# Kernel tuning notes

Hardware: AMD Instinct MI355X
Metric: run time of the kernel (lower is better)

Reference implementation:

```python
import jax, jax.numpy as jnp
import numpy as np

BLOCK = 16
NVFP4_LEVELS = jnp.array([0.0, 0.5, 1.0, 1.5, 2.0, 3.0, 4.0, 6.0], dtype=jnp.float32)


def _quantize_to_nvfp4(x_blocks):
    # x_blocks: [n_blocks, BLOCK]
    amax = jnp.clip(jnp.max(jnp.abs(x_blocks), axis=-1, keepdims=True), 1e-12, None)
    scale = amax / 6.0
    x_norm = jnp.abs(x_blocks) / scale
    idx = jnp.argmin(jnp.abs(x_norm[..., None] - NVFP4_LEVELS), axis=-1)
    return jnp.sign(x_blocks) * NVFP4_LEVELS[idx] * scale


def setup_inputs() -> dict:
    key = jax.random.key(0)
    k1, k2, k3, k4 = jax.random.split(key, 4)
    B, S, H, O = 16, 1024, 1152, 4608
    x = jax.random.normal(k1, (B, S, H), dtype=jnp.float32)
    w_quantized = jax.random.normal(k2, (O, H), dtype=jnp.float32) * 0.02
    smooth_scale = jax.random.uniform(k3, (H,), dtype=jnp.float32, minval=0.5, maxval=2.0)
    bias = jax.random.normal(k4, (O,), dtype=jnp.float32) * 0.02
    return {"x": x, "w_quantized": w_quantized, "smooth_scale": smooth_scale, "bias": bias}


def reference(x, w_quantized, smooth_scale, bias):
    orig_shape = x.shape
    H = orig_shape[-1]
    # SmoothQuant activation prescale
    x_s = (x * smooth_scale).reshape(-1, H)              # [T, H]
    # per-token prescale to [-6, 6]
    token_max = jnp.clip(jnp.max(jnp.abs(x_s), axis=-1, keepdims=True), 1e-12, None)
    pre_scale = token_max / 6.0
    x_pre = x_s / pre_scale
    # blockwise NVFP4 fake quant
    x_q = _quantize_to_nvfp4(x_pre.reshape(-1, BLOCK)).reshape(x_s.shape)
    x_q = x_q * pre_scale                                # restore token scale
    out = x_q.reshape(orig_shape) @ w_quantized.T + bias  # F.linear
    return out
```

## Files before the change

### kernel.cpp

```cpp
#include <hip/hip_runtime.h>
#include <hip/hip_bf16.h>

typedef __attribute__((ext_vector_type(8))) _Float16 f16x8;
typedef __attribute__((ext_vector_type(4))) float  f32x4;

#define H_DIM 1152
#define H_VEC (H_DIM / 4)

__device__ __forceinline__ float nvfp4_level(float xn) {
    return xn <= 0.25f ? 0.0f
         : xn <= 0.75f ? 0.5f
         : xn <= 1.25f ? 1.0f
         : xn <= 1.75f ? 1.5f
         : xn <= 2.5f  ? 2.0f
         : xn <= 3.5f  ? 3.0f
         : xn <= 5.0f  ? 4.0f : 6.0f;
}

__global__ __launch_bounds__(256) void quant_kernel(
    const float4* __restrict__ x4, const float4* __restrict__ s4,
    _Float16* __restrict__ xq)
{
    const int t    = (blockIdx.x << 2) + (threadIdx.x >> 6);
    const int lane = threadIdx.x & 63;
    const float4* xrow = x4 + (size_t)t * H_VEC;

    float4 v[5];
    int    fidx[5];
    float  m = 0.f;
    #pragma unroll
    for (int i = 0; i < 5; ++i) {
        const int f = (i < 4) ? (lane + 64 * i) : (256 + (lane & 31));
        fidx[i] = f;
        const float4 xx = xrow[f];
        const float4 ss = s4[f];
        float4 vv;
        vv.x = xx.x * ss.x; vv.y = xx.y * ss.y;
        vv.z = xx.z * ss.z; vv.w = xx.w * ss.w;
        v[i] = vv;
        m = fmaxf(m, fmaxf(fmaxf(fabsf(vv.x), fabsf(vv.y)),
                           fmaxf(fabsf(vv.z), fabsf(vv.w))));
    }
    #pragma unroll
    for (int off = 32; off; off >>= 1)
        m = fmaxf(m, __shfl_xor(m, off, 64));
    const float pre_scale = fmaxf(m, 1e-12f) / 6.0f;

    #pragma unroll
    for (int i = 0; i < 5; ++i) {
        float4 p;
        p.x = v[i].x / pre_scale;
        p.y = v[i].y / pre_scale;
        p.z = v[i].z / pre_scale;
        p.w = v[i].w / pre_scale;
        float g = fmaxf(fmaxf(fabsf(p.x), fabsf(p.y)),
                        fmaxf(fabsf(p.z), fabsf(p.w)));
        g = fmaxf(g, __shfl_xor(g, 1, 64));
        g = fmaxf(g, __shfl_xor(g, 2, 64));
        const float scale = fmaxf(g, 1e-12f) / 6.0f;

        alignas(8) _Float16 o[4];
        {
            float q;
            q = copysignf(nvfp4_level(fabsf(p.x) / scale) * scale, p.x) * pre_scale;
            o[0] = (_Float16)q;
            q = copysignf(nvfp4_level(fabsf(p.y) / scale) * scale, p.y) * pre_scale;
            o[1] = (_Float16)q;
            q = copysignf(nvfp4_level(fabsf(p.z) / scale) * scale, p.z) * pre_scale;
            o[2] = (_Float16)q;
            q = copysignf(nvfp4_level(fabsf(p.w) / scale) * scale, p.w) * pre_scale;
            o[3] = (_Float16)q;
        }
        if (i < 4 || lane < 32) {
            _Float16* dst = xq + (size_t)t * H_DIM + fidx[i] * 4;
            *(uint2*)dst = *(const uint2*)o;
        }
    }
}

__global__ __launch_bounds__(256) void wconv_kernel(
    const float* __restrict__ w, _Float16* __restrict__ wq, int n)
{
    int i = (blockIdx.x * 256 + threadIdx.x) * 4;
    if (i < n) {
        float4 v = *(const float4*)(w + i);
        alignas(8) _Float16 o[4];
        o[0] = (_Float16)v.x;
        o[1] = (_Float16)v.y;
        o[2] = (_Float16)v.z;
        o[3] = (_Float16)v.w;
        *(uint2*)(wq + i) = *(const uint2*)o;
    }
}

__device__ __forceinline__ void async_copy16(const void* gptr, void* lptr)
{
    __builtin_amdgcn_global_load_lds(
        (const __attribute__((address_space(1))) unsigned int*)gptr,
        (__attribute__((address_space(3))) unsigned int*)lptr,
        16, 0, 0);
}

#define BM 256
#define BN 256
#define BK 64

__global__ __launch_bounds__(512, 2) void gemm_bt_kernel(
    const _Float16* __restrict__ A,
    const _Float16* __restrict__ B,
    const float* __restrict__ bias,
    float* __restrict__ C,
    int M, int N, int K)
{
    __shared__ alignas(16) _Float16 sA[2][BM * BK];
    __shared__ alignas(16) _Float16 sB[2][BN * BK];

    const int tid    = threadIdx.x;
    const int wave   = tid >> 6;
    const int lane   = tid & 63;
    const int lane16 = lane & 15;
    const int quad   = lane >> 4;

    const int nbx = gridDim.x;
    const int nwg = nbx * gridDim.y;
    int bid = blockIdx.y * nbx + blockIdx.x;
    if ((nwg & 7) == 0) {
        const int cpx = nwg >> 3;
        bid = (bid & 7) * cpx + (bid >> 3);
    }
    const int m0 = (bid / nbx) * BM;
    const int n0 = (bid % nbx) * BN;

    const int wr = wave >> 2;
    const int wc = wave & 3;
    const int NT = K / BK;

    int srcA[4], srcB[4], ldst[4];
    #pragma unroll
    for (int s = 0; s < 4; ++s) {
        const int base = (wave * 4 + s) * 64;
        const int c    = base + lane;
        const int r    = c >> 3;
        const int sw   = ((c & 7) * 8) ^ ((r & 7) << 3);
        srcA[s] = (m0 + r) * K + sw;
        srcB[s] = (n0 + r) * K + sw;
        ldst[s] = base * 16;
    }

    auto stage = [&](int t, int d) {
        const int k0 = t * BK;
        #pragma unroll
        for (int s = 0; s < 4; ++s) {
            async_copy16(A + srcA[s] + k0, (char*)(&sA[d][0]) + ldst[s]);
            async_copy16(B + srcB[s] + k0, (char*)(&sB[d][0]) + ldst[s]);
        }
    };

    const int xr = (lane16 & 7) << 3;

    stage(0, 0);
    if (NT > 1) stage(1, 1);
    asm volatile("s_waitcnt vmcnt(8)" ::: "memory");
    __builtin_amdgcn_s_barrier();
    asm volatile("" ::: "memory");

    f32x4 acc[8][4] = {};

    for (int t = 0; t < NT; ++t) {
        const int d = t & 1;
        const _Float16* tA = &sA[d][0];
        const _Float16* tB = &sB[d][0];

        f16x8 b[4][2];
        f16x8 a[2][2][2];

        #pragma unroll
        for (int j = 0; j < 4; ++j) {
            const int rb = wc * 64 + j * 16 + lane16;
            #pragma unroll
            for (int ks = 0; ks < 2; ++ks)
                b[j][ks] = *(const f16x8*)(tB + rb * 64 + ((ks * 32 + quad * 8) ^ xr));
        }
        #pragma unroll
        for (int ii = 0; ii < 2; ++ii) {
            const int r = wr * 128 + ii * 16 + lane16;
            #pragma unroll
            for (int ks = 0; ks < 2; ++ks)
                a[0][ii][ks] = *(const f16x8*)(tA + r * 64 + ((ks * 32 + quad * 8) ^ xr));
        }

        #pragma unroll
        for (int p = 0; p < 4; ++p) {
            if (p < 3) {
                #pragma unroll
                for (int ii = 0; ii < 2; ++ii) {
                    const int r = wr * 128 + ((p + 1) * 2 + ii) * 16 + lane16;
                    #pragma unroll
                    for (int ks = 0; ks < 2; ++ks)
                        a[(p + 1) & 1][ii][ks] =
                            *(const f16x8*)(tA + r * 64 + ((ks * 32 + quad * 8) ^ xr));
                }
            } else {
                asm volatile("s_waitcnt lgkmcnt(0)" ::: "memory");
            }
            __builtin_amdgcn_s_barrier();
            if (p == 3) {
                asm volatile("" ::: "memory");
                if (t + 2 < NT) stage(t + 2, d);
            }
            __builtin_amdgcn_s_setprio(1);
            #pragma unroll
            for (int ii = 0; ii < 2; ++ii)
                #pragma unroll
                for (int j = 0; j < 4; ++j)
                    #pragma unroll
                    for (int ks = 0; ks < 2; ++ks)
                        acc[p * 2 + ii][j] = __builtin_amdgcn_mfma_f32_16x16x32_f16(
                            a[p & 1][ii][ks], b[j][ks], acc[p * 2 + ii][j], 0, 0, 0);
            __builtin_amdgcn_s_setprio(0);
        }

        if (t + 2 < NT) asm volatile("s_waitcnt vmcnt(8)" ::: "memory");
        else            asm volatile("s_waitcnt vmcnt(0)" ::: "memory");
        __builtin_amdgcn_s_barrier();
        asm volatile("" ::: "memory");
    }

    #pragma unroll
    for (int i = 0; i < 8; ++i) {
        const int m = m0 + wr * 128 + i * 16 + quad * 4;
        #pragma unroll
        for (int j = 0; j < 4; ++j) {
            const int n = n0 + wc * 64 + j * 16 + lane16;
            const float bv = bias[n];
            float* cp = C + (size_t)m * N + n;
            #pragma unroll
            for (int r2 = 0; r2 < 4; ++r2)
                cp[(size_t)r2 * N] = acc[i][j][r2] + bv;
        }
    }
}

extern "C" void kernel_launch(void* const* d_in, const int* in_sizes, int n_in,
                              void* d_out, int out_size, void* d_ws, size_t ws_size,
                              hipStream_t stream)
{
    const float* x      = (const float*)d_in[0];
    const float* w      = (const float*)d_in[1];
    const float* smooth = (const float*)d_in[2];
    const float* bias   = (const float*)d_in[3];
    float* out = (float*)d_out;

    const int H = in_sizes[2];
    const int T = in_sizes[0] / H;
    const int O = in_sizes[3];

    _Float16* xq = (_Float16*)d_ws;
    _Float16* wq = (_Float16*)((char*)d_ws + (size_t)T * H * sizeof(_Float16));

    quant_kernel<<<T / 4, 256, 0, stream>>>((const float4*)x, (const float4*)smooth, xq);
    wconv_kernel<<<(O * H / 4 + 255) / 256, 256, 0, stream>>>(w, wq, O * H);

    dim3 grid(O / BN, T / BM);
    gemm_bt_kernel<<<grid, 512, 0, stream>>>(xq, wq, bias, out, T, O, H);
}
```

Baseline: 556.9 us.

## Interleave half-tile async loads and prefetch next tile fragments in GEMM

Rewrites the GEMM main loop so the global-to-LDS copies for tile t+2 are split into B-halves and A-halves and issued across different MFMA phases, instead of all at once after the last phase. The B fragments and the first A fragments of the next tile are now read from LDS during the last phase of the current tile, so the LDS read latency at the start of each iteration overlaps with compute. The aim is to spread memory traffic more evenly and hide LDS and global latency behind MFMA work. In exchange it adds more workgroup barriers per iteration and makes the wait/barrier ordering more delicate.

```diff
diff --git a/kernel.cpp b/kernel.cpp
--- a/kernel.cpp
+++ b/kernel.cpp
@@ -135,95 +135,124 @@
     const int wc = wave & 3;
     const int NT = K / BK;
 
-    int srcA[4], srcB[4], ldst[4];
-    #pragma unroll
-    for (int s = 0; s < 4; ++s) {
-        const int base = (wave * 4 + s) * 64;
-        const int c    = base + lane;
-        const int r    = c >> 3;
-        const int sw   = ((c & 7) * 8) ^ ((r & 7) << 3);
-        srcA[s] = (m0 + r) * K + sw;
-        srcB[s] = (n0 + r) * K + sw;
-        ldst[s] = base * 16;
-    }
-
-    auto stage = [&](int t, int d) {
-        const int k0 = t * BK;
-        #pragma unroll
-        for (int s = 0; s < 4; ++s) {
-            async_copy16(A + srcA[s] + k0, (char*)(&sA[d][0]) + ldst[s]);
-            async_copy16(B + srcB[s] + k0, (char*)(&sB[d][0]) + ldst[s]);
-        }
+    int srcA[2][2], srcB[2][2], lofs[2][2];
+    #pragma unroll
+    for (int h = 0; h < 2; ++h)
+        #pragma unroll
+        for (int s = 0; s < 2; ++s) {
+            const int cb = (wave * 2 + s) * 64;
+            const int cu = cb + lane;
+            const int rl = cu >> 3;
+            const int sw = ((cu & 7) * 8) ^ ((rl & 7) << 3);
+            srcA[h][s] = (m0 + h * 128 + rl) * K + sw;
+            srcB[h][s] = (n0 + h * 128 + rl) * K + sw;
+            lofs[h][s] = (h * 1024 + cb) * 16;
+        }
+
+    auto stageA = [&](int tt, int dd, int h) {
+        const int k0 = tt * BK;
+        #pragma unroll
+        for (int s = 0; s < 2; ++s)
+            async_copy16(A + srcA[h][s] + k0, (char*)(&sA[dd][0]) + lofs[h][s]);
+    };
+    auto stageB = [&](int tt, int dd, int h) {
+        const int k0 = tt * BK;
+        #pragma unroll
+        for (int s = 0; s < 2; ++s)
+            async_copy16(B + srcB[h][s] + k0, (char*)(&sB[dd][0]) + lofs[h][s]);
     };
 
     const int xr = (lane16 & 7) << 3;
 
-    stage(0, 0);
-    if (NT > 1) stage(1, 1);
+    f16x8 aR0[2][2], aR1[2][2];
+    f16x8 b[4][2];
+    f32x4 acc[8][4] = {};
+
+    auto readA0 = [&](const _Float16* tA, int qd) {
+        #pragma unroll
+        for (int ii = 0; ii < 2; ++ii) {
+            const int r = wr * 128 + (qd * 2 + ii) * 16 + lane16;
+            #pragma unroll
+            for (int ks = 0; ks < 2; ++ks)
+                aR0[ii][ks] = *(const f16x8*)(tA + r * 64 + ((ks * 32 + quad * 8) ^ xr));
+        }
+    };
+    auto readA1 = [&](const _Float16* tA, int qd) {
+        #pragma unroll
+        for (int ii = 0; ii < 2; ++ii) {
+            const int r = wr * 128 + (qd * 2 + ii) * 16 + lane16;
+            #pragma unroll
+            for (int ks = 0; ks < 2; ++ks)
+                aR1[ii][ks] = *(const f16x8*)(tA + r * 64 + ((ks * 32 + quad * 8) ^ xr));
+        }
+    };
+    auto readB = [&](const _Float16* tB) {
+        #pragma unroll
+        for (int j = 0; j < 4; ++j) {
+            const int rb = wc * 64 + j * 16 + lane16;
+            #pragma unroll
+            for (int ks = 0; ks < 2; ++ks)
+                b[j][ks] = *(const f16x8*)(tB + rb * 64 + ((ks * 32 + quad * 8) ^ xr));
+        }
+    };
+
+#define MFMA_Q(q, AR) do {                                                        \
+    __builtin_amdgcn_s_setprio(1);                                                \
+    _Pragma("unroll")                                                             \
+    for (int ii = 0; ii < 2; ++ii)                                                \
+        _Pragma("unroll")                                                         \
+        for (int j = 0; j < 4; ++j)                                               \
+            _Pragma("unroll")                                                     \
+            for (int ks = 0; ks < 2; ++ks)                                        \
+                acc[(q) * 2 + ii][j] = __builtin_amdgcn_mfma_f32_16x16x32_f16(    \
+                    AR[ii][ks], b[j][ks], acc[(q) * 2 + ii][j], 0, 0, 0);         \
+    __builtin_amdgcn_s_setprio(0);                                                \
+} while (0)
+
+    stageB(0, 0, 0); stageB(0, 0, 1); stageA(0, 0, 0); stageA(0, 0, 1);
+    stageB(1, 1, 0); stageB(1, 1, 1); stageA(1, 1, 0); stageA(1, 1, 1);
     asm volatile("s_waitcnt vmcnt(8)" ::: "memory");
     __builtin_amdgcn_s_barrier();
     asm volatile("" ::: "memory");
-
-    f32x4 acc[8][4] = {};
+    readB(&sB[0][0]);
+    readA0(&sA[0][0], 0);
 
     for (int t = 0; t < NT; ++t) {
         const int d = t & 1;
         const _Float16* tA = &sA[d][0];
-        const _Float16* tB = &sB[d][0];
-
-        f16x8 b[4][2];
-        f16x8 a[2][2][2];
-
-        #pragma unroll
-        for (int j = 0; j < 4; ++j) {
-            const int rb = wc * 64 + j * 16 + lane16;
-            #pragma unroll
-            for (int ks = 0; ks < 2; ++ks)
-                b[j][ks] = *(const f16x8*)(tB + rb * 64 + ((ks * 32 + quad * 8) ^ xr));
-        }
-        #pragma unroll
-        for (int ii = 0; ii < 2; ++ii) {
-            const int r = wr * 128 + ii * 16 + lane16;
-            #pragma unroll
-            for (int ks = 0; ks < 2; ++ks)
-                a[0][ii][ks] = *(const f16x8*)(tA + r * 64 + ((ks * 32 + quad * 8) ^ xr));
-        }
-
-        #pragma unroll
-        for (int p = 0; p < 4; ++p) {
-            if (p < 3) {
-                #pragma unroll
-                for (int ii = 0; ii < 2; ++ii) {
-                    const int r = wr * 128 + ((p + 1) * 2 + ii) * 16 + lane16;
-                    #pragma unroll
-                    for (int ks = 0; ks < 2; ++ks)
-                        a[(p + 1) & 1][ii][ks] =
-                            *(const f16x8*)(tA + r * 64 + ((ks * 32 + quad * 8) ^ xr));
-                }
-            } else {
-                asm volatile("s_waitcnt lgkmcnt(0)" ::: "memory");
-            }
-            __builtin_amdgcn_s_barrier();
-            if (p == 3) {
-                asm volatile("" ::: "memory");
-                if (t + 2 < NT) stage(t + 2, d);
-            }
-            __builtin_amdgcn_s_setprio(1);
-            #pragma unroll
-            for (int ii = 0; ii < 2; ++ii)
-                #pragma unroll
-                for (int j = 0; j < 4; ++j)
-                    #pragma unroll
-                    for (int ks = 0; ks < 2; ++ks)
-                        acc[p * 2 + ii][j] = __builtin_amdgcn_mfma_f32_16x16x32_f16(
-                            a[p & 1][ii][ks], b[j][ks], acc[p * 2 + ii][j], 0, 0, 0);
-            __builtin_amdgcn_s_setprio(0);
-        }
-
-        if (t + 2 < NT) asm volatile("s_waitcnt vmcnt(8)" ::: "memory");
-        else            asm volatile("s_waitcnt vmcnt(0)" ::: "memory");
+        const bool pf = (t + 2 < NT);
+
+        readA1(tA, 1);
+        __builtin_amdgcn_s_barrier();
+        asm volatile("s_waitcnt lgkmcnt(0)" ::: "memory");
+        MFMA_Q(0, aR0);
+        __builtin_amdgcn_s_barrier();
+
+        readA0(tA, 2);
+        if (pf) stageB(t + 2, d, 0);
+        __builtin_amdgcn_s_barrier();
+        asm volatile("s_waitcnt lgkmcnt(0)" ::: "memory");
+        MFMA_Q(1, aR1);
+        __builtin_amdgcn_s_barrier();
+
+        readA1(tA, 3);
+        if (pf) stageB(t + 2, d, 1);
+        __builtin_amdgcn_s_barrier();
+        asm volatile("s_waitcnt lgkmcnt(0)" ::: "memory");
+        MFMA_Q(2, aR0);
+        __builtin_amdgcn_s_barrier();
+
+        if (pf) { stageA(t + 2, d, 0); stageA(t + 2, d, 1); }
+        if (pf) asm volatile("s_waitcnt vmcnt(8)" ::: "memory");
+        else    asm volatile("s_waitcnt vmcnt(0)" ::: "memory");
         __builtin_amdgcn_s_barrier();
         asm volatile("" ::: "memory");
+        MFMA_Q(3, aR1);
+        if (t + 1 < NT) {
+            readB(&sB[d ^ 1][0]);
+            readA0(&sA[d ^ 1][0], 0);
+        }
+        __builtin_amdgcn_s_barrier();
     }
 
     #pragma unroll
@@ -239,6 +268,7 @@
                 cp[(size_t)r2 * N] = acc[i][j][r2] + bv;
         }
     }
+#undef MFMA_Q
 }
 
 extern "C" void kernel_launch(void* const* d_in, const int* in_sizes, int n_in,
```

Result: no change. 547.7 us (-1.7%).
